# Kernel tuning notes

Measured on AMD Instinct MI355X. Metric: run time of the kernel, lower is better.

The kernel has to match this reference:

```python
import jax, jax.numpy as jnp
import numpy as np

IN_F, H1, H2, NC = 784, 1024, 1024, 10
BATCH = 32
EPS = 0.1


def setup_inputs() -> dict:
    key = jax.random.key(0)
    ks = jax.random.split(key, 8)
    x = jax.random.normal(ks[0], (BATCH, IN_F), jnp.float32)
    y = jax.random.randint(ks[1], (BATCH,), 0, NC)
    W1 = jax.random.normal(ks[2], (H1, IN_F), jnp.float32) / np.float32(np.sqrt(IN_F))
    b1 = jax.random.normal(ks[3], (H1,), jnp.float32) * 0.01
    W2 = jax.random.normal(ks[4], (H2, H1), jnp.float32) / np.float32(np.sqrt(H1))
    b2 = jax.random.normal(ks[5], (H2,), jnp.float32) * 0.01
    W3 = jax.random.normal(ks[6], (NC, H2), jnp.float32) / np.float32(np.sqrt(H2))
    b3 = jax.random.normal(ks[7], (NC,), jnp.float32) * 0.01
    return dict(x=x, y=y, W1=W1, b1=b1, W2=W2, b2=b2, W3=W3, b3=b3)


def _relu_coeffs(zl, zu):
    # d = 1 where zl>=0, zu/(zu-zl) where crossing, 0 where zu<=0 (as in select_layer)
    I = (zl < 0) & (zu > 0)
    d = jnp.where(zl >= 0, 1.0, jnp.where(I, zu / (zu - zl), 0.0))
    lI = jnp.where(I, zl, 0.0)  # zl restricted to crossing set I
    return d, lI


def reference(x, y, W1, b1, W2, b2, W3, b3):
    eps = jnp.float32(EPS)
    # ---- layer-1 preactivation bounds (InfBall fval) ----
    nom1 = x @ W1.T + b1                              # [B,H1]
    r1 = eps * jnp.abs(W1).sum(1)                     # [H1]
    zl1, zu1 = nom1 - r1, nom1 + r1
    d1, l1m = _relu_coeffs(zl1, zu1)                  # [B,H1]

    # ---- layer-2 preactivation bounds via dual (transpose) propagation, nu = I ----
    nu1 = W2[None, :, :] * d1[:, None, :]             # [B,H2,H1]  (D1 W2^T rows)
    V0 = jnp.einsum('bji,ik->bjk', nu1, W1)           # [B,H2,IN]
    A = jnp.einsum('bjk,bk->bj', V0, x) + b2 + nu1 @ b1
    E = eps * jnp.abs(V0).sum(-1)
    crossl = jnp.einsum('bji,bi->bj', jax.nn.relu(-nu1), l1m)
    crossu = jnp.einsum('bji,bi->bj', jax.nn.relu(nu1), l1m)
    zl2 = A - E + crossl
    zu2 = A + E - crossu
    d2, l2m = _relu_coeffs(zl2, zu2)                  # [B,H2]

    # ---- final robust bounds: c[b,j,:] = e_{y_b} - e_j ----
    eye = jnp.eye(NC, dtype=x.dtype)
    c = eye[y][:, None, :] - eye[None, :, :]          # [B,NC,NC]
    nu2 = (c @ W3) * d2[:, None, :]                   # [B,NC,H2]
    nu1f = (nu2 @ W2) * d1[:, None, :]                # [B,NC,H1]
    V0f = nu1f @ W1                                   # [B,NC,IN]
    Af = jnp.einsum('bjk,bk->bj', V0f, x) + c @ b3 + nu2 @ b2 + nu1f @ b1
    Ef = eps * jnp.abs(V0f).sum(-1)
    crossf = (jnp.einsum('bji,bi->bj', jax.nn.relu(-nu2), l2m)
              + jnp.einsum('bji,bi->bj', jax.nn.relu(-nu1f), l1m))
    J = Af - Ef + crossf                              # lower bound of c^T z
    return -J                                         # f: upper bound of z_j - z_y, [B,NC]
```

## Files before the change

### kernel.cpp

```cpp
#include <hip/hip_runtime.h>
#include <math.h>

#define B    32
#define INF  784
#define H1   1024
#define H2   1024
#define NC   10
#define EPSV 0.1f

typedef __attribute__((ext_vector_type(8))) short short8;
typedef __attribute__((ext_vector_type(4))) float floatx4;

__device__ inline ushort bf16_rne(float f) {
  uint u = __builtin_bit_cast(uint, f);
  u += 0x7FFFu + ((u >> 16) & 1u);
  return (ushort)(u >> 16);
}
__device__ inline uint pack2(float a, float b) {
  return (uint)bf16_rne(a) | ((uint)bf16_rne(b) << 16);
}
__device__ inline uint scale_pack(uint u, float d0, float d1v) {
  float f0 = __builtin_bit_cast(float, u << 16) * d0;
  float f1 = __builtin_bit_cast(float, u & 0xFFFF0000u) * d1v;
  uint r0 = __builtin_bit_cast(uint, f0) + 0x8000u;
  uint r1 = __builtin_bit_cast(uint, f1) + 0x8000u;
  return __builtin_amdgcn_perm(r1, r0, 0x07060302u);
}

typedef __attribute__((address_space(1))) const unsigned int g_as1;
typedef __attribute__((address_space(3))) unsigned int l_as3;
__device__ __forceinline__ void gll16(const void* g, void* l) {
  __builtin_amdgcn_global_load_lds((g_as1*)g, (l_as3*)l, 16, 0, 0);
}

__global__ __launch_bounds__(256) void k_pre(
    const float* __restrict__ x, const float* __restrict__ W1,
    const float* __restrict__ b1, const float* __restrict__ W2,
    ushort* __restrict__ W1F, ushort* __restrict__ W2F,
    float* __restrict__ d1B, float* __restrict__ t1B, float* __restrict__ dnB,
    float* __restrict__ Ezero)
{
  __shared__ float red[4][B + 1];
  __shared__ float Ts[4][32][17];
  int bid = blockIdx.x;
  int t = threadIdx.x;
  if (bid < 64) {
    int jt = bid;
    int lane = t & 63, c0 = t >> 6;
    int l15 = lane & 15, quad = lane >> 4;
    for (int c = c0; c < 32; c += 4) {
      const float* src = &W2[(size_t)(jt * 16 + l15) * H1 + c * 32 + quad * 8];
      float4 v0 = *reinterpret_cast<const float4*>(src);
      float4 v1 = *reinterpret_cast<const float4*>(src + 4);
      uint4 o;
      o.x = pack2(v0.x, v0.y); o.y = pack2(v0.z, v0.w);
      o.z = pack2(v1.x, v1.y); o.w = pack2(v1.z, v1.w);
      *reinterpret_cast<uint4*>(&W2F[((size_t)(c * 64 + jt) * 64 + lane) * 8]) = o;
    }
  } else if (bid < 116) {
    int mt = bid - 64;
    int w = t >> 6, lane = t & 63;
    int l15 = lane & 15, quad = lane >> 4;
    if (mt >= 49) {
      uint4 z; z.x = 0; z.y = 0; z.z = 0; z.w = 0;
      for (int cg = 0; cg < 8; cg++) {
        int c = cg * 4 + w;
        *reinterpret_cast<uint4*>(&W1F[((size_t)(c * 52 + mt) * 64 + lane) * 8]) = z;
      }
    } else {
      int col0 = mt * 16;
      for (int cg = 0; cg < 8; cg++) {
        int c = cg * 4 + w;
#pragma unroll
        for (int p = 0; p < 8; p++) {
          int r = p * 4 + (lane >> 4);
          Ts[w][r][lane & 15] = W1[(size_t)(c * 32 + r) * INF + col0 + (lane & 15)];
        }
        float f[8];
#pragma unroll
        for (int e = 0; e < 8; e++) f[e] = Ts[w][quad * 8 + e][l15];
        uint4 o;
        o.x = pack2(f[0], f[1]); o.y = pack2(f[2], f[3]);
        o.z = pack2(f[4], f[5]); o.w = pack2(f[6], f[7]);
        *reinterpret_cast<uint4*>(&W1F[((size_t)(c * 52 + mt) * 64 + lane) * 8]) = o;
      }
    }
  } else if (bid < 1140) {
    int i = bid - 116;
    const float* w = W1 + (size_t)i * INF;
    float acc[B];
#pragma unroll
    for (int b = 0; b < B; b++) acc[b] = 0.f;
    float wabs = 0.f;
    for (int k = t; k < INF; k += 256) {
      float wv = w[k];
      wabs += fabsf(wv);
#pragma unroll
      for (int b = 0; b < B; b++) acc[b] = fmaf(x[b * INF + k], wv, acc[b]);
    }
#pragma unroll
    for (int off = 32; off > 0; off >>= 1) {
#pragma unroll
      for (int b = 0; b < B; b++) acc[b] += __shfl_down(acc[b], off, 64);
      wabs += __shfl_down(wabs, off, 64);
    }
    int wave = t >> 6, lane = t & 63;
    if (lane == 0) {
#pragma unroll
      for (int b = 0; b < B; b++) red[wave][b] = acc[b];
      red[wave][B] = wabs;
    }
    __syncthreads();
    if (t < B) {
      float s = red[0][t] + red[1][t] + red[2][t] + red[3][t];
      float r = EPSV * (red[0][B] + red[1][B] + red[2][B] + red[3][B]);
      float nom = s + b1[i];
      float zl = nom - r, zu = nom + r;
      float d, l;
      if (zl >= 0.f)      { d = 1.f;            l = 0.f; }
      else if (zu > 0.f)  { d = zu / (zu - zl); l = zl;  }
      else                { d = 0.f;            l = 0.f; }
      d1B[(size_t)t * H1 + i] = d;
      t1B[(size_t)t * H1 + i] = d * l;
      dnB[(size_t)t * H1 + i] = d * nom;
    }
  } else {
    int zb = bid - 1140;
    for (int idx = t; idx < 8192; idx += 256) {
      int pos = zb * 8192 + idx;
      if (pos < 54272) Ezero[pos] = 0.f;
    }
  }
}

#define K3_ISSUE(c, buf) do {                                                   \
  for (int mi = w; mi < 13; mi += 4)                                            \
    gll16(W1F + (((size_t)(c) * 52 + mtBase + mi) * 64 + lane) * 8,             \
          &Abuf[buf][mi * 64]);                                                 \
} while (0)

#define K3_SCALE(bv, DsRow, cc, bfr) do {                                       \
  float4 dv0 = *reinterpret_cast<const float4*>(&DsRow[(cc) * 32]);             \
  float4 dv1 = *reinterpret_cast<const float4*>(&DsRow[(cc) * 32 + 4]);         \
  uint4 sb;                                                                     \
  sb.x = scale_pack(bv.x, dv0.x, dv0.y);                                        \
  sb.y = scale_pack(bv.y, dv0.z, dv0.w);                                        \
  sb.z = scale_pack(bv.z, dv1.x, dv1.y);                                        \
  sb.w = scale_pack(bv.w, dv1.z, dv1.w);                                        \
  bfr = __builtin_bit_cast(short8, sb);                                         \
} while (0)

#define K3_MFMA(buf, bf0, bf1) do {                                             \
  _Pragma("unroll")                                                             \
  for (int mi = 0; mi < 13; mi++) {                                             \
    short8 af = *reinterpret_cast<const short8*>(&Abuf[buf][mi * 64 + lane]);   \
    acc[0][mi] = __builtin_amdgcn_mfma_f32_16x16x32_bf16(af, bf0, acc[0][mi], 0, 0, 0); \
    acc[1][mi] = __builtin_amdgcn_mfma_f32_16x16x32_bf16(af, bf1, acc[1][mi], 0, 0, 0); \
  }                                                                             \
} while (0)

__global__ __launch_bounds__(256, 3) void k3(
    const ushort* __restrict__ W1F, const ushort* __restrict__ W2F,
    const float* __restrict__ d1B, float* __restrict__ E)
{
  int b0 = blockIdx.z * 2;
  int t = threadIdx.x, w = t >> 6, lane = t & 63;
  int quad = lane >> 4, l15 = lane & 15;
  int jt = blockIdx.y * 4 + w;
  int mtBase = blockIdx.x * 13;

  __shared__ float Ds[2][H1];
  __shared__ uint4 Abuf[2][13 * 64];

  for (int idx = t; idx < 2 * H1; idx += 256)
    Ds[idx >> 10][idx & 1023] = d1B[(size_t)(b0 + (idx >> 10)) * H1 + (idx & 1023)];

  const ushort* bBase = W2F + ((size_t)jt * 64 + lane) * 8;
  const float* Ds0 = &Ds[0][quad * 8];
  const float* Ds1 = &Ds[1][quad * 8];

  floatx4 acc[2][13];
#pragma unroll
  for (int bb = 0; bb < 2; bb++)
#pragma unroll
    for (int mi = 0; mi < 13; mi++) acc[bb][mi] = (floatx4){0.f, 0.f, 0.f, 0.f};

  K3_ISSUE(0, 0);
  uint4 bv0 = *reinterpret_cast<const uint4*>(bBase);
  uint4 bv1 = *reinterpret_cast<const uint4*>(bBase + 32768);
  __syncthreads();

  for (int c = 0; c < 32; c += 2) {
    if (c + 1 < 32) K3_ISSUE(c + 1, 1);
    {
      short8 bf0, bf1;
      K3_SCALE(bv0, Ds0, c, bf0);
      K3_SCALE(bv0, Ds1, c, bf1);
      if (c + 2 < 32) bv0 = *reinterpret_cast<const uint4*>(bBase + (size_t)(c + 2) * 32768);
      K3_MFMA(0, bf0, bf1);
    }
    __syncthreads();
    if (c + 2 < 32) K3_ISSUE(c + 2, 0);
    {
      short8 bf0, bf1;
      K3_SCALE(bv1, Ds0, c + 1, bf0);
      K3_SCALE(bv1, Ds1, c + 1, bf1);
      if (c + 3 < 32) bv1 = *reinterpret_cast<const uint4*>(bBase + (size_t)(c + 3) * 32768);
      K3_MFMA(1, bf0, bf1);
    }
    __syncthreads();
  }

#pragma unroll
  for (int bb = 0; bb < 2; bb++) {
    float s = 0.f;
#pragma unroll
    for (int mi = 0; mi < 13; mi++)
#pragma unroll
      for (int r = 0; r < 4; r++) s += fabsf(acc[bb][mi][r]);
    s += __shfl_xor(s, 16, 64);
    s += __shfl_xor(s, 32, 64);
    if (lane < 16) {
      int j = jt * 16 + l15;
      atomicAdd(&E[(size_t)j * B + b0 + bb], EPSV * s);
    }
  }
}

__global__ __launch_bounds__(256) void k245a(
    const float* __restrict__ W2, const float* __restrict__ b2,
    const float* __restrict__ dnB, const float* __restrict__ t1B,
    const float* __restrict__ E, const float* __restrict__ W3,
    const int* __restrict__ y,
    float* __restrict__ nu2T, float* __restrict__ F2)
{
  int j = blockIdx.x;
  int t = threadIdx.x;
  int wave = t >> 6, lane = t & 63;
  int b0 = wave * 8;
  float aA[8] = {}, aCl[8] = {}, aCu[8] = {};
  const float* __restrict__ w2 = W2 + (size_t)j * H1;
  for (int i = lane; i < H1; i += 64) {
    float wv = w2[i];
    float wp = fmaxf(wv, 0.f), wn = fmaxf(-wv, 0.f);
#pragma unroll
    for (int r = 0; r < 8; r++) {
      float dv = dnB[(size_t)(b0 + r) * H1 + i];
      float tv = t1B[(size_t)(b0 + r) * H1 + i];
      aA[r]  = fmaf(wv, dv, aA[r]);
      aCl[r] = fmaf(wn, tv, aCl[r]);
      aCu[r] = fmaf(wp, tv, aCu[r]);
    }
  }
#pragma unroll
  for (int off = 32; off > 0; off >>= 1) {
#pragma unroll
    for (int r = 0; r < 8; r++) {
      aA[r]  += __shfl_down(aA[r],  off, 64);
      aCl[r] += __shfl_down(aCl[r], off, 64);
      aCu[r] += __shfl_down(aCu[r], off, 64);
    }
  }
  __shared__ float sA[B], sCl[B], sCu[B];
  __shared__ float sd2[B], st2[B], sdb[B], swy[B], sw3[NC];
  float bj = b2[j];
  if (lane == 0) {
#pragma unroll
    for (int r = 0; r < 8; r++) {
      sA [b0 + r] = aA[r] + bj;
      sCl[b0 + r] = aCl[r];
      sCu[b0 + r] = aCu[r];
    }
  }
  if (t >= 64 && t < 96)   swy[t - 64]  = W3[(size_t)y[t - 64] * H2 + j];
  if (t >= 128 && t < 138) sw3[t - 128] = W3[(size_t)(t - 128) * H2 + j];
  __syncthreads();
  if (t < B) {
    float a = sA[t], e = E[(size_t)j * B + t];
    float zl = a - e + sCl[t];
    float zu = a + e - sCu[t];
    float d, l;
    if (zl >= 0.f)      { d = 1.f;            l = 0.f; }
    else if (zu > 0.f)  { d = zu / (zu - zl); l = zl;  }
    else                { d = 0.f;            l = 0.f; }
    sd2[t] = d;
    st2[t] = d * l;
    sdb[t] = d * bj;
  }
  __syncthreads();
  for (int tt = t; tt < B * NC; tt += 256) {
    int b = tt / NC, jc = tt - b * NC;
    float cw = swy[b] - sw3[jc];
    float d2v = sd2[b];
    nu2T[((size_t)b * H2 + j) * 12 + jc] = cw * d2v;
    float val = cw * sdb[b] + fmaxf(-cw, 0.f) * st2[b];
    atomicAdd(&F2[((size_t)(j & 63) * B + b) * NC + jc], val);
  }
}

__global__ __launch_bounds__(256) void k5b1(
    const float* __restrict__ W2, const float* __restrict__ nu2T,
    float* __restrict__ hpart)
{
  int t = threadIdx.x;
  int i1 = blockIdx.x * 512 + t * 2;
  int b = blockIdx.y, s = blockIdx.z;
  const float* __restrict__ nrowb = nu2T + ((size_t)b * H2 + s * 128) * 12;
  const float* __restrict__ w2b = W2 + (size_t)s * 128 * H1 + i1;
  float h0[NC] = {}, h1[NC] = {};
  for (int i2 = 0; i2 < 128; i2++) {
    float2 wv = *reinterpret_cast<const float2*>(&w2b[(size_t)i2 * H1]);
    const float* __restrict__ nrow = nrowb + i2 * 12;
#pragma unroll
    for (int j = 0; j < NC; j++) {
      h0[j] = fmaf(nrow[j], wv.x, h0[j]);
      h1[j] = fmaf(nrow[j], wv.y, h1[j]);
    }
  }
#pragma unroll
  for (int j = 0; j < NC; j++) {
    float2 o; o.x = h0[j]; o.y = h1[j];
    *reinterpret_cast<float2*>(&hpart[(((size_t)s * B + b) * NC + j) * H1 + i1]) = o;
  }
}

__global__ __launch_bounds__(256) void k5b2(
    const float* __restrict__ hpart,
    const float* __restrict__ d1B, const float* __restrict__ t1B,
    const float* __restrict__ dnB,
    float* __restrict__ nu1fT, float* __restrict__ F)
{
  int t = threadIdx.x;
  int i1 = blockIdx.x * 256 + t;
  int b = blockIdx.y;
  float d1v = d1B[(size_t)b * H1 + i1];
  float t1v = t1B[(size_t)b * H1 + i1];
  float dnv = dnB[(size_t)b * H1 + i1];
  float sn[NC], c1[NC];
#pragma unroll
  for (int j = 0; j < NC; j++) {
    float hv = 0.f;
#pragma unroll
    for (int s = 0; s < 8; s++)
      hv += hpart[(((size_t)s * B + b) * NC + j) * H1 + i1];
    nu1fT[((size_t)b * H1 + i1) * 12 + j] = hv * d1v;
    sn[j] = hv * dnv;
    c1[j] = fmaxf(-hv, 0.f) * t1v;
  }
#pragma unroll
  for (int off = 32; off > 0; off >>= 1) {
#pragma unroll
    for (int j = 0; j < NC; j++) {
      sn[j] += __shfl_down(sn[j], off, 64);
      c1[j] += __shfl_down(c1[j], off, 64);
    }
  }
  __shared__ float red[4][2 * NC];
  int wave = t >> 6, lane = t & 63;
  if (lane == 0) {
#pragma unroll
    for (int j = 0; j < NC; j++) { red[wave][j] = sn[j]; red[wave][NC + j] = c1[j]; }
  }
  __syncthreads();
  if (t < NC) {
    float s = 0.f;
    for (int w = 0; w < 4; w++) s += red[w][t] + red[w][NC + t];
    atomicAdd(&F[b * NC + t], s);
  }
}

__global__ __launch_bounds__(128) void k5c1(
    const float* __restrict__ W1, const float* __restrict__ nu1fT,
    float* __restrict__ ppart)
{
  int t = threadIdx.x;
  bool valid = (t < 112);
  int k = blockIdx.x * 112 + (valid ? t : 0);
  int b = blockIdx.y, s = blockIdx.z;
  const float* __restrict__ nrowb = nu1fT + ((size_t)b * H1 + s * 128) * 12;
  const float* __restrict__ w1b = W1 + (size_t)s * 128 * INF + k;
  float acc[NC] = {};
  for (int i1 = 0; i1 < 128; i1++) {
    float w1v = w1b[(size_t)i1 * INF];
    const float* __restrict__ nrow = nrowb + i1 * 12;
#pragma unroll
    for (int j = 0; j < NC; j++) acc[j] = fmaf(nrow[j], w1v, acc[j]);
  }
  if (valid) {
#pragma unroll
    for (int j = 0; j < NC; j++)
      ppart[(((size_t)s * B + b) * NC + j) * INF + k] = acc[j];
  }
}

__global__ __launch_bounds__(256) void k5c2_out(
    const float* __restrict__ ppart, const float* __restrict__ F,
    const float* __restrict__ F2, const float* __restrict__ b3,
    const int* __restrict__ y, float* __restrict__ out)
{
  int b = blockIdx.x;
  int t = threadIdx.x;
  float e[NC] = {};
  for (int k = t; k < INF; k += 256) {
#pragma unroll
    for (int j = 0; j < NC; j++) {
      float v = 0.f;
#pragma unroll
      for (int s = 0; s < 8; s++)
        v += ppart[(((size_t)s * B + b) * NC + j) * INF + k];
      e[j] += fabsf(v);
    }
  }
#pragma unroll
  for (int off = 32; off > 0; off >>= 1) {
#pragma unroll
    for (int j = 0; j < NC; j++) e[j] += __shfl_down(e[j], off, 64);
  }
  __shared__ float red[4][NC];
  int wave = t >> 6, lane = t & 63;
  if (lane == 0) {
#pragma unroll
    for (int j = 0; j < NC; j++) red[wave][j] = e[j];
  }
  __syncthreads();
  if (t < NC) {
    float ef = 0.f;
    for (int w = 0; w < 4; w++) ef += red[w][t];
    float s = F[b * NC + t];
    for (int slot = 0; slot < 64; slot++)
      s += F2[((size_t)slot * B + b) * NC + t];
    int yb = y[b];
    s += b3[yb] - b3[t];
    out[b * NC + t] = EPSV * ef - s;
  }
}

extern "C" void kernel_launch(void* const* d_in, const int* in_sizes, int n_in,
                              void* d_out, int out_size, void* d_ws, size_t ws_size,
                              hipStream_t stream) {
  const float* x  = (const float*)d_in[0];
  const int*   y  = (const int*)  d_in[1];
  const float* W1 = (const float*)d_in[2];
  const float* b1 = (const float*)d_in[3];
  const float* W2 = (const float*)d_in[4];
  const float* b2 = (const float*)d_in[5];
  const float* W3 = (const float*)d_in[6];
  const float* b3 = (const float*)d_in[7];
  float* out = (float*)d_out;
  float* ws  = (float*)d_ws;

  float* d1B  = ws;
  float* t1B  = ws + 32768;
  float* dnB  = ws + 65536;
  float* E    = ws + 196608;
  float* F    = ws + 229376;
  float* F2   = ws + 230400;
  float* nu2T = ws + 328704;
  ushort* W2F = (ushort*)(ws + 721920);
  ushort* W1F = (ushort*)(ws + 1246208);
  float* nu1fT = ws + 328704;
  float* hpart = ws + 721920;
  float* ppart = ws + 721920;

  k_pre<<<1147, 256, 0, stream>>>(x, W1, b1, W2, W1F, W2F, d1B, t1B, dnB, E);
  k3<<<dim3(4, 16, 16), 256, 0, stream>>>(W1F, W2F, d1B, E);
  k245a<<<H2, 256, 0, stream>>>(W2, b2, dnB, t1B, E, W3, y, nu2T, F2);
  k5b1<<<dim3(2, B, 8), 256, 0, stream>>>(W2, nu2T, hpart);
  k5b2<<<dim3(4, B), 256, 0, stream>>>(hpart, d1B, t1B, dnB, nu1fT, F);
  k5c1<<<dim3(7, B, 8), 128, 0, stream>>>(W1, nu1fT, ppart);
  k5c2_out<<<B, 256, 0, stream>>>(ppart, F, F2, b3, y, out);
}
```

Baseline: 216.6 us.

## Load k3 A-tiles straight to registers and parallelize the final reduction

The k3 GEMM now reads W1F fragments directly from global memory into registers instead of staging them through double-buffered LDS. This removes the per-step __syncthreads barriers, but each of the four waves now fetches the same A data on its own. The M tiling drops from 13 to 10 tiles per block, with W1F padded to 50 tiles and 5 blocks along x, which lowers register pressure and adds more blocks. The last stage is split into a 2-D grid reduction kernel that accumulates |V0f| sums with atomics into a zeroed buffer, followed by a tiny kernel that writes the output, replacing the previous 32-block serial loop.

```diff
diff --git a/kernel.cpp b/kernel.cpp
--- a/kernel.cpp
+++ b/kernel.cpp
@@ -27,13 +27,7 @@
   return __builtin_amdgcn_perm(r1, r0, 0x07060302u);
 }
 
-typedef __attribute__((address_space(1))) const unsigned int g_as1;
-typedef __attribute__((address_space(3))) unsigned int l_as3;
-__device__ __forceinline__ void gll16(const void* g, void* l) {
-  __builtin_amdgcn_global_load_lds((g_as1*)g, (l_as3*)l, 16, 0, 0);
-}
-
-__global__ __launch_bounds__(256) void k_pre(
+__global__ __launch_bounds__(256) void k_pre50(
     const float* __restrict__ x, const float* __restrict__ W1,
     const float* __restrict__ b1, const float* __restrict__ W2,
     ushort* __restrict__ W1F, ushort* __restrict__ W2F,
@@ -57,7 +51,7 @@
       o.z = pack2(v1.x, v1.y); o.w = pack2(v1.z, v1.w);
       *reinterpret_cast<uint4*>(&W2F[((size_t)(c * 64 + jt) * 64 + lane) * 8]) = o;
     }
-  } else if (bid < 116) {
+  } else if (bid < 114) {
     int mt = bid - 64;
     int w = t >> 6, lane = t & 63;
     int l15 = lane & 15, quad = lane >> 4;
@@ -65,7 +59,7 @@
       uint4 z; z.x = 0; z.y = 0; z.z = 0; z.w = 0;
       for (int cg = 0; cg < 8; cg++) {
         int c = cg * 4 + w;
-        *reinterpret_cast<uint4*>(&W1F[((size_t)(c * 52 + mt) * 64 + lane) * 8]) = z;
+        *reinterpret_cast<uint4*>(&W1F[((size_t)(c * 50 + mt) * 64 + lane) * 8]) = z;
       }
     } else {
       int col0 = mt * 16;
@@ -82,11 +76,11 @@
         uint4 o;
         o.x = pack2(f[0], f[1]); o.y = pack2(f[2], f[3]);
         o.z = pack2(f[4], f[5]); o.w = pack2(f[6], f[7]);
-        *reinterpret_cast<uint4*>(&W1F[((size_t)(c * 52 + mt) * 64 + lane) * 8]) = o;
+        *reinterpret_cast<uint4*>(&W1F[((size_t)(c * 50 + mt) * 64 + lane) * 8]) = o;
       }
     }
-  } else if (bid < 1140) {
-    int i = bid - 116;
+  } else if (bid < 1138) {
+    int i = bid - 114;
     const float* w = W1 + (size_t)i * INF;
     float acc[B];
 #pragma unroll
@@ -125,35 +119,42 @@
       dnB[(size_t)t * H1 + i] = d * nom;
     }
   } else {
-    int zb = bid - 1140;
+    int zb = bid - 1138;
     for (int idx = t; idx < 8192; idx += 256) {
       int pos = zb * 8192 + idx;
-      if (pos < 54272) Ezero[pos] = 0.f;
-    }
-  }
-}
-
-#define K3_ISSUE(c, buf) do {                                                   \
-  for (int mi = w; mi < 13; mi += 4)                                            \
-    gll16(W1F + (((size_t)(c) * 52 + mtBase + mi) * 64 + lane) * 8,             \
-          &Abuf[buf][mi * 64]);                                                 \
+      if (pos < 55296) Ezero[pos] = 0.f;
+    }
+  }
+}
+
+#define K3_LOADA(c) do {                                                        \
+  _Pragma("unroll")                                                             \
+  for (int mi = 0; mi < 10; mi++)                                               \
+    a[mi] = *reinterpret_cast<const uint4*>(aBase + (size_t)(c) * 25600 + mi * 512); \
 } while (0)
 
-#define K3_SCALE(bv, DsRow, cc, bfr) do {                                       \
-  float4 dv0 = *reinterpret_cast<const float4*>(&DsRow[(cc) * 32]);             \
-  float4 dv1 = *reinterpret_cast<const float4*>(&DsRow[(cc) * 32 + 4]);         \
-  uint4 sb;                                                                     \
-  sb.x = scale_pack(bv.x, dv0.x, dv0.y);                                        \
-  sb.y = scale_pack(bv.y, dv0.z, dv0.w);                                        \
-  sb.z = scale_pack(bv.z, dv1.x, dv1.y);                                        \
-  sb.w = scale_pack(bv.w, dv1.z, dv1.w);                                        \
-  bfr = __builtin_bit_cast(short8, sb);                                         \
+#define K3_SCALE2(bv, bf0, bf1, cc) do {                                        \
+  float4 d00 = *reinterpret_cast<const float4*>(&Ds0[(cc) * 32]);               \
+  float4 d01 = *reinterpret_cast<const float4*>(&Ds0[(cc) * 32 + 4]);           \
+  float4 d10 = *reinterpret_cast<const float4*>(&Ds1[(cc) * 32]);               \
+  float4 d11 = *reinterpret_cast<const float4*>(&Ds1[(cc) * 32 + 4]);           \
+  uint4 s0, s1;                                                                 \
+  s0.x = scale_pack(bv.x, d00.x, d00.y);                                        \
+  s0.y = scale_pack(bv.y, d00.z, d00.w);                                        \
+  s0.z = scale_pack(bv.z, d01.x, d01.y);                                        \
+  s0.w = scale_pack(bv.w, d01.z, d01.w);                                        \
+  s1.x = scale_pack(bv.x, d10.x, d10.y);                                        \
+  s1.y = scale_pack(bv.y, d10.z, d10.w);                                        \
+  s1.z = scale_pack(bv.z, d11.x, d11.y);                                        \
+  s1.w = scale_pack(bv.w, d11.z, d11.w);                                        \
+  bf0 = __builtin_bit_cast(short8, s0);                                         \
+  bf1 = __builtin_bit_cast(short8, s1);                                         \
 } while (0)
 
-#define K3_MFMA(buf, bf0, bf1) do {                                             \
+#define K3_MFMA(bf0, bf1) do {                                                  \
   _Pragma("unroll")                                                             \
-  for (int mi = 0; mi < 13; mi++) {                                             \
-    short8 af = *reinterpret_cast<const short8*>(&Abuf[buf][mi * 64 + lane]);   \
+  for (int mi = 0; mi < 10; mi++) {                                             \
+    short8 af = __builtin_bit_cast(short8, a[mi]);                              \
     acc[0][mi] = __builtin_amdgcn_mfma_f32_16x16x32_bf16(af, bf0, acc[0][mi], 0, 0, 0); \
     acc[1][mi] = __builtin_amdgcn_mfma_f32_16x16x32_bf16(af, bf1, acc[1][mi], 0, 0, 0); \
   }                                                                             \
@@ -166,56 +167,50 @@
   int b0 = blockIdx.z * 2;
   int t = threadIdx.x, w = t >> 6, lane = t & 63;
   int quad = lane >> 4, l15 = lane & 15;
+  int mt0 = blockIdx.x * 10;
   int jt = blockIdx.y * 4 + w;
-  int mtBase = blockIdx.x * 13;
 
   __shared__ float Ds[2][H1];
-  __shared__ uint4 Abuf[2][13 * 64];
-
   for (int idx = t; idx < 2 * H1; idx += 256)
     Ds[idx >> 10][idx & 1023] = d1B[(size_t)(b0 + (idx >> 10)) * H1 + (idx & 1023)];
-
+  __syncthreads();
+
+  const ushort* aBase = W1F + ((size_t)mt0 * 64 + lane) * 8;
   const ushort* bBase = W2F + ((size_t)jt * 64 + lane) * 8;
   const float* Ds0 = &Ds[0][quad * 8];
   const float* Ds1 = &Ds[1][quad * 8];
 
-  floatx4 acc[2][13];
+  floatx4 acc[2][10];
 #pragma unroll
   for (int bb = 0; bb < 2; bb++)
 #pragma unroll
-    for (int mi = 0; mi < 13; mi++) acc[bb][mi] = (floatx4){0.f, 0.f, 0.f, 0.f};
-
-  K3_ISSUE(0, 0);
+    for (int mi = 0; mi < 10; mi++) acc[bb][mi] = (floatx4){0.f, 0.f, 0.f, 0.f};
+
+  uint4 a[10];
   uint4 bv0 = *reinterpret_cast<const uint4*>(bBase);
   uint4 bv1 = *reinterpret_cast<const uint4*>(bBase + 32768);
-  __syncthreads();
-
   for (int c = 0; c < 32; c += 2) {
-    if (c + 1 < 32) K3_ISSUE(c + 1, 1);
+    K3_LOADA(c);
     {
       short8 bf0, bf1;
-      K3_SCALE(bv0, Ds0, c, bf0);
-      K3_SCALE(bv0, Ds1, c, bf1);
+      K3_SCALE2(bv0, bf0, bf1, c);
       if (c + 2 < 32) bv0 = *reinterpret_cast<const uint4*>(bBase + (size_t)(c + 2) * 32768);
-      K3_MFMA(0, bf0, bf1);
-    }
-    __syncthreads();
-    if (c + 2 < 32) K3_ISSUE(c + 2, 0);
+      K3_MFMA(bf0, bf1);
+    }
+    K3_LOADA(c + 1);
     {
       short8 bf0, bf1;
-      K3_SCALE(bv1, Ds0, c + 1, bf0);
-      K3_SCALE(bv1, Ds1, c + 1, bf1);
+      K3_SCALE2(bv1, bf0, bf1, c + 1);
       if (c + 3 < 32) bv1 = *reinterpret_cast<const uint4*>(bBase + (size_t)(c + 3) * 32768);
-      K3_MFMA(1, bf0, bf1);
-    }
-    __syncthreads();
+      K3_MFMA(bf0, bf1);
+    }
   }
 
 #pragma unroll
   for (int bb = 0; bb < 2; bb++) {
     float s = 0.f;
 #pragma unroll
-    for (int mi = 0; mi < 13; mi++)
+    for (int mi = 0; mi < 10; mi++)
 #pragma unroll
       for (int r = 0; r < 4; r++) s += fabsf(acc[bb][mi][r]);
     s += __shfl_xor(s, 16, 64);
@@ -393,45 +388,50 @@
   }
 }
 
-__global__ __launch_bounds__(256) void k5c2_out(
-    const float* __restrict__ ppart, const float* __restrict__ F,
+__global__ __launch_bounds__(128) void k5c2p(
+    const float* __restrict__ ppart, float* __restrict__ EfB)
+{
+  int t = threadIdx.x;
+  bool valid = (t < 112);
+  int k = blockIdx.x * 112 + (valid ? t : 0);
+  int b = blockIdx.y;
+  float e[NC];
+#pragma unroll
+  for (int j = 0; j < NC; j++) {
+    float v = 0.f;
+#pragma unroll
+    for (int s = 0; s < 8; s++)
+      v += ppart[(((size_t)s * B + b) * NC + j) * INF + k];
+    e[j] = valid ? fabsf(v) : 0.f;
+  }
+#pragma unroll
+  for (int off = 32; off > 0; off >>= 1) {
+#pragma unroll
+    for (int j = 0; j < NC; j++) e[j] += __shfl_down(e[j], off, 64);
+  }
+  __shared__ float red[2][NC];
+  int wave = t >> 6, lane = t & 63;
+  if (lane == 0) {
+#pragma unroll
+    for (int j = 0; j < NC; j++) red[wave][j] = e[j];
+  }
+  __syncthreads();
+  if (t < NC) atomicAdd(&EfB[b * NC + t], red[0][t] + red[1][t]);
+}
+
+__global__ __launch_bounds__(320) void k_out(
+    const float* __restrict__ EfB, const float* __restrict__ F,
     const float* __restrict__ F2, const float* __restrict__ b3,
     const int* __restrict__ y, float* __restrict__ out)
 {
-  int b = blockIdx.x;
-  int t = threadIdx.x;
-  float e[NC] = {};
-  for (int k = t; k < INF; k += 256) {
-#pragma unroll
-    for (int j = 0; j < NC; j++) {
-      float v = 0.f;
-#pragma unroll
-      for (int s = 0; s < 8; s++)
-        v += ppart[(((size_t)s * B + b) * NC + j) * INF + k];
-      e[j] += fabsf(v);
-    }
-  }
-#pragma unroll
-  for (int off = 32; off > 0; off >>= 1) {
-#pragma unroll
-    for (int j = 0; j < NC; j++) e[j] += __shfl_down(e[j], off, 64);
-  }
-  __shared__ float red[4][NC];
-  int wave = t >> 6, lane = t & 63;
-  if (lane == 0) {
-#pragma unroll
-    for (int j = 0; j < NC; j++) red[wave][j] = e[j];
-  }
-  __syncthreads();
-  if (t < NC) {
-    float ef = 0.f;
-    for (int w = 0; w < 4; w++) ef += red[w][t];
-    float s = F[b * NC + t];
+  int t = threadIdx.x;
+  if (t < B * NC) {
+    int b = t / NC, j = t - b * NC;
+    float s = F[b * NC + j];
     for (int slot = 0; slot < 64; slot++)
-      s += F2[((size_t)slot * B + b) * NC + t];
-    int yb = y[b];
-    s += b3[yb] - b3[t];
-    out[b * NC + t] = EPSV * ef - s;
+      s += F2[((size_t)slot * B + b) * NC + j];
+    s += b3[y[b]] - b3[j];
+    out[b * NC + j] = EPSV * EfB[b * NC + j] - s;
   }
 }
 
@@ -455,6 +455,7 @@
   float* E    = ws + 196608;
   float* F    = ws + 229376;
   float* F2   = ws + 230400;
+  float* EfB  = ws + 250880;
   float* nu2T = ws + 328704;
   ushort* W2F = (ushort*)(ws + 721920);
   ushort* W1F = (ushort*)(ws + 1246208);
@@ -462,11 +463,12 @@
   float* hpart = ws + 721920;
   float* ppart = ws + 721920;
 
-  k_pre<<<1147, 256, 0, stream>>>(x, W1, b1, W2, W1F, W2F, d1B, t1B, dnB, E);
-  k3<<<dim3(4, 16, 16), 256, 0, stream>>>(W1F, W2F, d1B, E);
+  k_pre50<<<1145, 256, 0, stream>>>(x, W1, b1, W2, W1F, W2F, d1B, t1B, dnB, E);
+  k3<<<dim3(5, 16, 16), 256, 0, stream>>>(W1F, W2F, d1B, E);
   k245a<<<H2, 256, 0, stream>>>(W2, b2, dnB, t1B, E, W3, y, nu2T, F2);
   k5b1<<<dim3(2, B, 8), 256, 0, stream>>>(W2, nu2T, hpart);
   k5b2<<<dim3(4, B), 256, 0, stream>>>(hpart, d1B, t1B, dnB, nu1fT, F);
   k5c1<<<dim3(7, B, 8), 128, 0, stream>>>(W1, nu1fT, ppart);
-  k5c2_out<<<B, 256, 0, stream>>>(ppart, F, F2, b3, y, out);
-}
+  k5c2p<<<dim3(7, B), 128, 0, stream>>>(ppart, EfB);
+  k_out<<<1, 320, 0, stream>>>(EfB, F, F2, b3, y, out);
+}
```

Result: no change. 212.6 us (-1.8%).
